# Kernel optimization log

Measured on AMD Instinct MI355X. Metric: run time of the kernel, lower is better.

Reference implementation:

```python
import jax, jax.numpy as jnp
import numpy as np

# Grid / model dims (from init_kwargs)
B, C, XD, YD = 32, 16, 128, 128      # batch, channels, X_dim, Y_dim
XW, YW = 4, 4                        # window
H, Wd = XD // XW, YD // YW
F = XW * YW * C                      # 256 features per cell
R = 512                              # rnn_size


def setup_inputs() -> dict:
    key = jax.random.key(0)
    k1, k2, k3 = jax.random.split(key, 3)
    x = jax.random.normal(k1, (B, C, XD, YD), dtype=jnp.float32)
    # torch.nn.Linear default init: U(-1/sqrt(fan_in), 1/sqrt(fan_in))
    s = 1.0 / float(np.sqrt(F + 2 * R))
    W = jax.random.uniform(k2, (F + 2 * R, 5 * R), jnp.float32, -s, s)
    b = jax.random.uniform(k3, (5 * R,), jnp.float32, -s, s)
    return {"x": x, "W": W, "b": b}


def _mdlstm(x, W, b):
    # [B,C,XD,YD] -> [B,XD,YD,C] -> [B,H,W,F] -> [H,W,B,F] (same raw reshape as torch .view)
    xg = jnp.transpose(x, (0, 2, 3, 1)).reshape(B, H, Wd, F)
    xg = jnp.transpose(xg, (1, 2, 0, 3))
    zeros = jnp.zeros((B, R), x.dtype)

    def cell(xi, c_up, h_up, c_left, h_left):
        # concat order matches torch: (inputs, h1=up, h2=left); split i,j,f1,f2,o
        z = jnp.concatenate([xi, h_up, h_left], axis=-1) @ W + b
        i, j, f1, f2, o = jnp.split(z, 5, axis=-1)
        # forget_bias = 0.0
        nc = (c_up * jax.nn.sigmoid(f1)
              + c_left * jax.nn.sigmoid(f2)
              + jax.nn.sigmoid(i) * jnp.tanh(j))
        nh = jnp.tanh(nc) * jax.nn.sigmoid(o)
        return nc, nh

    # Row-by-row scan is mathematically identical to the diagonal wavefront:
    # each cell depends only on its up and left neighbors.
    def row_step(carry, xrow):
        c_up_row, h_up_row = carry            # [W,B,R] each
        def col_step(left, inp):
            c_l, h_l = left
            xi, c_u, h_u = inp
            nc, nh = cell(xi, c_u, h_u, c_l, h_l)
            return (nc, nh), (nc, nh)
        _, (cs, hs) = jax.lax.scan(col_step, (zeros, zeros), (xrow, c_up_row, h_up_row))
        return (cs, hs), hs

    init = (jnp.zeros((Wd, B, R), x.dtype), jnp.zeros((Wd, B, R), x.dtype))
    _, hs = jax.lax.scan(row_step, init, xg)   # [H,W,B,R]
    return jnp.transpose(hs, (2, 0, 1, 3))     # [B,H,W,R]


def reference(x, W, b):
    return _mdlstm(x, W, b)
```

## Files before the change

kernel.cpp:

```cpp
#include <hip/hip_runtime.h>


typedef _Float16 f16;
typedef f16   f16x8 __attribute__((ext_vector_type(8)));
typedef float f32x4 __attribute__((ext_vector_type(4)));

#define SCL (1.0f/1024.0f)

#define FLAGS_OFF  0L
#define FLAGS2_OFF 4096L
#define ZERO_OFF   40960L
#define BT_OFF     131072L
#define BT_BYTES   13107200L
#define XG_OFF     (BT_OFF + BT_BYTES)
#define XG_PLANE   8388608L
#define XG_BYTES   (XG_PLANE*4L)
#define HR_OFF     (XG_OFF + XG_BYTES)
#define HR_PLANE   1048576L
#define HR_BYTES   (HR_PLANE*4L)
#define CR_OFF     (HR_OFF + HR_BYTES)
#define CR_BYTES   (HR_PLANE*4L)

__global__ __launch_bounds__(256) void gather_xg_k(const float* __restrict__ x, f16* __restrict__ xg) {
  int cb = blockIdx.x;
  int f  = threadIdx.x;
  int cell = cb >> 5, b = cb & 31;
  int hh = cell >> 5, ww = cell & 31;
  int c  = f & 15, fo = f >> 4;
  int xd = hh*4 + (ww >> 3);
  int yd = (ww & 7)*16 + fo;
  float v = x[(((long)b*16 + c)*128 + xd)*128 + yd] * 16.0f;
  f16 hi = (f16)v;
  f16 lo = (f16)(v - (float)hi);
  long o = (long)cb*256 + f;
  xg[o] = hi;
  xg[XG_PLANE + o] = lo;
}

__global__ __launch_bounds__(256) void prep_b_k(const float* __restrict__ Wm, f16* __restrict__ Bt) {
  int idx = blockIdx.x*256 + threadIdx.x;
  int lane = idx & 63;
  int t    = idx >> 6;
  int kstep = t % 40, ntile = t / 40;
  int s = ntile / 5, g = ntile % 5;
  int n = g*512 + s*16 + (lane & 15);
  int k = kstep*32 + (lane >> 4)*8;
  f16x8 vh, vl;
#pragma unroll
  for (int u = 0; u < 8; ++u) {
    float w = Wm[(long)(k+u)*2560 + n] * 64.0f;
    f16 hi = (f16)w;
    vh[u] = hi;
    vl[u] = (f16)(w - (float)hi);
  }
  ((f16x8*)Bt)[(long)idx*2]     = vh;
  ((f16x8*)Bt)[(long)idx*2 + 1] = vl;
}

__device__ __forceinline__ float sigf(float x) { return 1.0f/(1.0f + __expf(-x)); }
__device__ __forceinline__ float tanh_fast(float x) {
  float e = __expf(-2.0f*fabsf(x));
  float t = (1.0f - e)/(1.0f + e);
  return x >= 0.0f ? t : -t;
}

__device__ __forceinline__ f16x8 ld_nt(const f16* p) {
  return __builtin_nontemporal_load((const f16x8*)p);
}
__device__ __forceinline__ float ld_ntf(const float* p) {
  return __builtin_nontemporal_load(p);
}
__device__ __forceinline__ void st_sc_f32(float* p, float v) {
  asm volatile("global_store_dword %0, %1, off sc0 sc1" :: "v"(p), "v"(v) : "memory");
}
__device__ __forceinline__ void st_sc_f16(f16* p, f16 v) {
  unsigned v32 = (unsigned)__builtin_bit_cast(unsigned short, v);
  asm volatile("global_store_short %0, %1, off sc0 sc1" :: "v"(p), "v"(v32) : "memory");
}

#define PREFA(PF, A0H, A0L, A1H, A1L)                                         \
  { const int pfa_ = (PF);                                                    \
    if (pfa_ < 8) {                                                           \
      const int o_ = pfa_*32 + l4*8;                                          \
      A0H = *(const f16x8*)(pxh + l15*256 + o_);                              \
      A0L = *(const f16x8*)(pxl + l15*256 + o_);                              \
      A1H = *(const f16x8*)(pxh + (16+l15)*256 + o_);                         \
      A1L = *(const f16x8*)(pxl + (16+l15)*256 + o_);                         \
    } else {                                                                  \
      const f16 *qh_, *ql_; int kl_;                                          \
      if (pfa_ < 24) { kl_ = (pfa_-8)*32;  qh_ = puh; ql_ = pul; }            \
      else           { kl_ = (pfa_-24)*32; qh_ = plh; ql_ = pll; }            \
      const int o_ = kl_ + l4*8;                                              \
      A0H = ld_nt(qh_ + l15*512 + o_);                                        \
      A0L = ld_nt(ql_ + l15*512 + o_);                                        \
      A1H = ld_nt(qh_ + (16+l15)*512 + o_);                                   \
      A1L = ld_nt(ql_ + (16+l15)*512 + o_);                                   \
    } }

#define PREFB(PF)                                                             \
  { const int pfb_ = (PF);                                                    \
    _Pragma("unroll")                                                         \
    for (int g = 0; g < 5; ++g) {                                             \
      const long b2_ = ((long)bfbase + g*2560 + pfb_*64)*2;                   \
      Bh[g] = Bf[b2_]; Bl[g] = Bf[b2_+1];                                     \
    } }

#define MFMAS(A0H, A0L, A1H, A1L)                                             \
  _Pragma("unroll")                                                           \
  for (int g = 0; g < 5; ++g) {                                               \
    acc[0][g] = __builtin_amdgcn_mfma_f32_16x16x32_f16(A0H, Bh[g], acc[0][g], 0,0,0); \
    acc[0][g] = __builtin_amdgcn_mfma_f32_16x16x32_f16(A0L, Bh[g], acc[0][g], 0,0,0); \
    acc[0][g] = __builtin_amdgcn_mfma_f32_16x16x32_f16(A0H, Bl[g], acc[0][g], 0,0,0); \
    acc[1][g] = __builtin_amdgcn_mfma_f32_16x16x32_f16(A1H, Bh[g], acc[1][g], 0,0,0); \
    acc[1][g] = __builtin_amdgcn_mfma_f32_16x16x32_f16(A1L, Bh[g], acc[1][g], 0,0,0); \
    acc[1][g] = __builtin_amdgcn_mfma_f32_16x16x32_f16(A1H, Bl[g], acc[1][g], 0,0,0); \
  }

__global__ __launch_bounds__(256, 3) void mdlstm_wave_k(
    const f16* __restrict__ Bt, const f16* __restrict__ xg,
    f16* __restrict__ hr, float* __restrict__ cr,
    const float* __restrict__ bias, const f16* __restrict__ zb,
    float* __restrict__ out, int* __restrict__ flags, int* __restrict__ flags2)
{
  const int wid = blockIdx.x;
  const int xcd = wid & 7, u = wid >> 3;
  const int subslice = u & 3, cellgroup = u >> 2;
  const int s = subslice*8 + xcd, r0 = s*16;
  const int grp6 = wid >> 7;
  const bool leader = (wid & 127) == 0;
  const int tid = threadIdx.x, wave = tid >> 6, lane = tid & 63;
  const int l15 = lane & 15, l4 = lane >> 4;
  const f16x8* __restrict__ Bf = (const f16x8*)Bt;
  const int bfbase = s*12800 + lane;
  const int kb = wave*10;

  __shared__ f32x4 lred[4][10][64];

  float bia[5];
#pragma unroll
  for (int g = 0; g < 5; ++g) bia[g] = bias[g*512 + r0 + l15];

  for (int d = 0; d < 63; ++d) {
    if (d > 0) {
      if (tid == 0) {
        if (leader) {
          while (__hip_atomic_load(&flags2[((d-1)*6 + grp6)*16], __ATOMIC_RELAXED, __HIP_MEMORY_SCOPE_AGENT) < 128)
            __builtin_amdgcn_s_sleep(1);
          __hip_atomic_fetch_add(&flags[d-1], 1, __ATOMIC_RELAXED, __HIP_MEMORY_SCOPE_AGENT);
        }
        while (__hip_atomic_load(&flags[d-1], __ATOMIC_RELAXED, __HIP_MEMORY_SCOPE_AGENT) < 6)
          __builtin_amdgcn_s_sleep(1);
      }
      __syncthreads();
    }
    const int ncell = (d < 32) ? (d + 1) : (63 - d);
    const int i0    = (d < 32) ? 0 : (d - 31);
    const int rprev = ((d-1)&1)*32;

#pragma unroll 1
    for (int rep = 0; rep < 2; ++rep) {
      const int L = cellgroup + rep*24;
      if (L >= ncell) break;

      const int i = i0 + L, j = d - i;
      const long cid = (long)i*32 + j;
      const f16 *pxh = xg + cid*8192, *pxl = xg + XG_PLANE + cid*8192;
      const f16 *puh = (i>0) ? (hr + (long)(rprev+i-1)*16384) : zb;
      const f16 *pul = (i>0) ? (hr + HR_PLANE + (long)(rprev+i-1)*16384) : zb;
      const f16 *plh = (j>0) ? (hr + (long)(rprev+i)*16384) : zb;
      const f16 *pll = (j>0) ? (hr + HR_PLANE + (long)(rprev+i)*16384) : zb;

      float cu_r[4], cl_r[4];
      if (wave < 2) {
#pragma unroll
        for (int v = 0; v < 4; ++v) {
          const int off = (wave*16 + l4*4 + v)*512 + r0 + l15;
          cu_r[v] = (i>0) ? ld_ntf(cr + (long)(rprev+i-1)*16384 + off) : 0.0f;
          cl_r[v] = (j>0) ? ld_ntf(cr + (long)(rprev+i)*16384 + off)   : 0.0f;
        }
      }

      f32x4 acc[2][5];
#pragma unroll
      for (int mt = 0; mt < 2; ++mt)
#pragma unroll
        for (int g = 0; g < 5; ++g) acc[mt][g] = (f32x4){0.f,0.f,0.f,0.f};

      f16x8 Bh[5], Bl[5];
      f16x8 c0h, c0l, c1h, c1l, n0h, n0l, n1h, n1l;
      PREFA(kb, c0h, c0l, c1h, c1l);
#pragma unroll
      for (int t = 0; t < 10; t += 2) {
        PREFA(kb+t+1, n0h, n0l, n1h, n1l);
        PREFB(kb+t);
        MFMAS(c0h, c0l, c1h, c1l);
        if (t+2 < 10) PREFA(kb+t+2, c0h, c0l, c1h, c1l);
        PREFB(kb+t+1);
        MFMAS(n0h, n0l, n1h, n1l);
      }

#pragma unroll
      for (int mt = 0; mt < 2; ++mt)
#pragma unroll
        for (int g = 0; g < 5; ++g)
          lred[wave][mt*5+g][lane] = acc[mt][g];
      __syncthreads();

      if (wave < 2) {
        f32x4 sum[5];
#pragma unroll
        for (int g = 0; g < 5; ++g)
          sum[g] = lred[0][wave*5+g][lane] + lred[1][wave*5+g][lane]
                 + lred[2][wave*5+g][lane] + lred[3][wave*5+g][lane];

        const long wb = (long)((d&1)*32 + i)*16384;
#pragma unroll
        for (int v = 0; v < 4; ++v) {
          const int brow = wave*16 + l4*4 + v;
          const int off = brow*512 + r0 + l15;
          float zi  = sum[0][v]*SCL + bia[0];
          float zj  = sum[1][v]*SCL + bia[1];
          float zf1 = sum[2][v]*SCL + bia[2];
          float zf2 = sum[3][v]*SCL + bia[3];
          float zo  = sum[4][v]*SCL + bia[4];
          float nc = cu_r[v]*sigf(zf1) + cl_r[v]*sigf(zf2) + sigf(zi)*tanh_fast(zj);
          float nh = tanh_fast(nc)*sigf(zo);
          st_sc_f32(cr + wb + off, nc);
          float nhs = nh * 16.0f;
          f16 hh = (f16)nhs;
          st_sc_f16(hr + wb + off, hh);
          st_sc_f16(hr + HR_PLANE + wb + off, (f16)(nhs - (float)hh));
          __builtin_nontemporal_store(nh, out + (((long)brow*32 + i)*32 + j)*512 + r0 + l15);
        }
      }
      __syncthreads();
    }

    asm volatile("s_waitcnt vmcnt(0)" ::: "memory");
    __syncthreads();
    if (tid == 0)
      __hip_atomic_fetch_add(&flags2[(d*6 + grp6)*16], 1, __ATOMIC_RELAXED, __HIP_MEMORY_SCOPE_AGENT);
  }
}

extern "C" void kernel_launch(void* const* d_in, const int* in_sizes, int n_in,
                              void* d_out, int out_size, void* d_ws, size_t ws_size,
                              hipStream_t stream) {
  const float* x  = (const float*)d_in[0];
  const float* Wm = (const float*)d_in[1];
  const float* bs = (const float*)d_in[2];
  float* out = (float*)d_out;
  char* ws = (char*)d_ws;

  int*   flags  = (int*)(ws + FLAGS_OFF);
  int*   flags2 = (int*)(ws + FLAGS2_OFF);
  f16*   zb     = (f16*)(ws + ZERO_OFF);
  f16*   Bt     = (f16*)(ws + BT_OFF);
  f16*   xgb    = (f16*)(ws + XG_OFF);
  f16*   hrb    = (f16*)(ws + HR_OFF);
  float* crb    = (float*)(ws + CR_OFF);

  hipMemsetAsync(ws, 0, BT_OFF, stream);
  gather_xg_k<<<32768, 256, 0, stream>>>(x, xgb);
  prep_b_k<<<1600, 256, 0, stream>>>(Wm, Bt);
  mdlstm_wave_k<<<768, 256, 0, stream>>>(Bt, xgb, hrb, crb, bs, zb, out, flags, flags2);
}
```

Measured before the change: 3.058 ms.

## Launch 1024 persistent blocks so each diagonal cell gets its own group

The persistent wavefront kernel grows from 768 to 1024 blocks (occupancy hint raised to 4 blocks per CU), so 32 cell groups cover every cell of a diagonal in one pass and the two-rep loop with its extra barrier goes away. The h buffer becomes a full per-cell array indexed by cell id instead of a two-diagonal ping-pong, and the up/left h loads drop their nontemporal hint so they may hit cache. Sync counters move from 6 to 8 groups and the spin sleep gets longer. Risks are register pressure from the higher occupancy target, a much larger workspace, and the assumption that all 1024 blocks are co-resident.

Result: slower. 3.263 ms (+6.7%).

```diff
diff --git a/kernel.cpp b/kernel.cpp
--- a/kernel.cpp
+++ b/kernel.cpp
@@ -16,10 +16,10 @@
 #define XG_PLANE   8388608L
 #define XG_BYTES   (XG_PLANE*4L)
 #define HR_OFF     (XG_OFF + XG_BYTES)
-#define HR_PLANE   1048576L
+#define HR_PLANE   16777216L
 #define HR_BYTES   (HR_PLANE*4L)
 #define CR_OFF     (HR_OFF + HR_BYTES)
-#define CR_BYTES   (HR_PLANE*4L)
+#define CR_BYTES   (2L*32*16384*4)
 
 __global__ __launch_bounds__(256) void gather_xg_k(const float* __restrict__ x, f16* __restrict__ xg) {
   int cb = blockIdx.x;
@@ -64,9 +64,6 @@
   return x >= 0.0f ? t : -t;
 }
 
-__device__ __forceinline__ f16x8 ld_nt(const f16* p) {
-  return __builtin_nontemporal_load((const f16x8*)p);
-}
 __device__ __forceinline__ float ld_ntf(const float* p) {
   return __builtin_nontemporal_load(p);
 }
@@ -91,10 +88,10 @@
       if (pfa_ < 24) { kl_ = (pfa_-8)*32;  qh_ = puh; ql_ = pul; }            \
       else           { kl_ = (pfa_-24)*32; qh_ = plh; ql_ = pll; }            \
       const int o_ = kl_ + l4*8;                                              \
-      A0H = ld_nt(qh_ + l15*512 + o_);                                        \
-      A0L = ld_nt(ql_ + l15*512 + o_);                                        \
-      A1H = ld_nt(qh_ + (16+l15)*512 + o_);                                   \
-      A1L = ld_nt(ql_ + (16+l15)*512 + o_);                                   \
+      A0H = *(const f16x8*)(qh_ + l15*512 + o_);                              \
+      A0L = *(const f16x8*)(ql_ + l15*512 + o_);                              \
+      A1H = *(const f16x8*)(qh_ + (16+l15)*512 + o_);                         \
+      A1L = *(const f16x8*)(ql_ + (16+l15)*512 + o_);                         \
     } }
 
 #define PREFB(PF)                                                             \
@@ -116,7 +113,7 @@
     acc[1][g] = __builtin_amdgcn_mfma_f32_16x16x32_f16(A1H, Bl[g], acc[1][g], 0,0,0); \
   }
 
-__global__ __launch_bounds__(256, 3) void mdlstm_wave_k(
+__global__ __launch_bounds__(256, 4) void mdlstm_wave_k(
     const f16* __restrict__ Bt, const f16* __restrict__ xg,
     f16* __restrict__ hr, float* __restrict__ cr,
     const float* __restrict__ bias, const f16* __restrict__ zb,
@@ -126,7 +123,7 @@
   const int xcd = wid & 7, u = wid >> 3;
   const int subslice = u & 3, cellgroup = u >> 2;
   const int s = subslice*8 + xcd, r0 = s*16;
-  const int grp6 = wid >> 7;
+  const int grp8 = wid >> 7;
   const bool leader = (wid & 127) == 0;
   const int tid = threadIdx.x, wave = tid >> 6, lane = tid & 63;
   const int l15 = lane & 15, l4 = lane >> 4;
@@ -144,31 +141,28 @@
     if (d > 0) {
       if (tid == 0) {
         if (leader) {
-          while (__hip_atomic_load(&flags2[((d-1)*6 + grp6)*16], __ATOMIC_RELAXED, __HIP_MEMORY_SCOPE_AGENT) < 128)
-            __builtin_amdgcn_s_sleep(1);
+          while (__hip_atomic_load(&flags2[((d-1)*8 + grp8)*16], __ATOMIC_RELAXED, __HIP_MEMORY_SCOPE_AGENT) < 128)
+            __builtin_amdgcn_s_sleep(2);
           __hip_atomic_fetch_add(&flags[d-1], 1, __ATOMIC_RELAXED, __HIP_MEMORY_SCOPE_AGENT);
         }
-        while (__hip_atomic_load(&flags[d-1], __ATOMIC_RELAXED, __HIP_MEMORY_SCOPE_AGENT) < 6)
-          __builtin_amdgcn_s_sleep(1);
+        while (__hip_atomic_load(&flags[d-1], __ATOMIC_RELAXED, __HIP_MEMORY_SCOPE_AGENT) < 8)
+          __builtin_amdgcn_s_sleep(2);
       }
       __syncthreads();
     }
     const int ncell = (d < 32) ? (d + 1) : (63 - d);
     const int i0    = (d < 32) ? 0 : (d - 31);
     const int rprev = ((d-1)&1)*32;
-
-#pragma unroll 1
-    for (int rep = 0; rep < 2; ++rep) {
-      const int L = cellgroup + rep*24;
-      if (L >= ncell) break;
-
+    const int L     = cellgroup;
+
+    if (L < ncell) {
       const int i = i0 + L, j = d - i;
       const long cid = (long)i*32 + j;
       const f16 *pxh = xg + cid*8192, *pxl = xg + XG_PLANE + cid*8192;
-      const f16 *puh = (i>0) ? (hr + (long)(rprev+i-1)*16384) : zb;
-      const f16 *pul = (i>0) ? (hr + HR_PLANE + (long)(rprev+i-1)*16384) : zb;
-      const f16 *plh = (j>0) ? (hr + (long)(rprev+i)*16384) : zb;
-      const f16 *pll = (j>0) ? (hr + HR_PLANE + (long)(rprev+i)*16384) : zb;
+      const f16 *puh = (i>0) ? (hr + (cid-32)*16384) : zb;
+      const f16 *pul = (i>0) ? (hr + HR_PLANE + (cid-32)*16384) : zb;
+      const f16 *plh = (j>0) ? (hr + (cid-1)*16384) : zb;
+      const f16 *pll = (j>0) ? (hr + HR_PLANE + (cid-1)*16384) : zb;
 
       float cu_r[4], cl_r[4];
       if (wave < 2) {
@@ -213,7 +207,8 @@
           sum[g] = lred[0][wave*5+g][lane] + lred[1][wave*5+g][lane]
                  + lred[2][wave*5+g][lane] + lred[3][wave*5+g][lane];
 
-        const long wb = (long)((d&1)*32 + i)*16384;
+        const long wbc = (long)((d&1)*32 + i)*16384;
+        const long wbh = cid*16384;
 #pragma unroll
         for (int v = 0; v < 4; ++v) {
           const int brow = wave*16 + l4*4 + v;
@@ -225,21 +220,20 @@
           float zo  = sum[4][v]*SCL + bia[4];
           float nc = cu_r[v]*sigf(zf1) + cl_r[v]*sigf(zf2) + sigf(zi)*tanh_fast(zj);
           float nh = tanh_fast(nc)*sigf(zo);
-          st_sc_f32(cr + wb + off, nc);
+          st_sc_f32(cr + wbc + off, nc);
           float nhs = nh * 16.0f;
           f16 hh = (f16)nhs;
-          st_sc_f16(hr + wb + off, hh);
-          st_sc_f16(hr + HR_PLANE + wb + off, (f16)(nhs - (float)hh));
+          st_sc_f16(hr + wbh + off, hh);
+          st_sc_f16(hr + HR_PLANE + wbh + off, (f16)(nhs - (float)hh));
           __builtin_nontemporal_store(nh, out + (((long)brow*32 + i)*32 + j)*512 + r0 + l15);
         }
       }
-      __syncthreads();
     }
 
     asm volatile("s_waitcnt vmcnt(0)" ::: "memory");
     __syncthreads();
     if (tid == 0)
-      __hip_atomic_fetch_add(&flags2[(d*6 + grp6)*16], 1, __ATOMIC_RELAXED, __HIP_MEMORY_SCOPE_AGENT);
+      __hip_atomic_fetch_add(&flags2[(d*8 + grp8)*16], 1, __ATOMIC_RELAXED, __HIP_MEMORY_SCOPE_AGENT);
   }
 }
 
@@ -263,5 +257,5 @@
   hipMemsetAsync(ws, 0, BT_OFF, stream);
   gather_xg_k<<<32768, 256, 0, stream>>>(x, xgb);
   prep_b_k<<<1600, 256, 0, stream>>>(Wm, Bt);
-  mdlstm_wave_k<<<768, 256, 0, stream>>>(Bt, xgb, hrb, crb, bs, zb, out, flags, flags2);
-}
+  mdlstm_wave_k<<<1024, 256, 0, stream>>>(Bt, xgb, hrb, crb, bs, zb, out, flags, flags2);
+}
```
